# Kernel optimization log

Hardware: AMD Instinct MI355X
Metric: run time of the kernel (lower is better)

## Reference

```python
import jax, jax.numpy as jnp
import numpy as np

B = 1024      # number of states
NP = 32       # SVGD particles per state
AD = 20       # act_dim
OD = 64       # obs_dim
H = 256       # critic hidden width
STEPS = 5     # num_svgd_steps
LR = 0.1      # svgd_lr (adaptive_lr disabled)
SP0 = 1.0     # svgd_sigma_p0
ALIM = 1.0    # act_limit


def _q(obs, X, w1, b1, w2, b2, w3, b3):
    h = jnp.concatenate([obs, X], axis=-1)
    h = jax.nn.relu(h @ w1 + b1)
    h = jax.nn.relu(h @ w2 + b2)
    return jnp.squeeze(h @ w3 + b3, -1)


def _rbf(X):
    # X: [B, NP, AD] -> K [B,NP,NP], diff [B,NP,NP,AD], gamma [B,1,1], K_grad [B,NP,NP,AD]
    diff = X[:, :, None, :] - X[:, None, :, :]
    dist_sq = jnp.sum(diff * diff, axis=-1)
    # adaptive bandwidth via median heuristic (adaptive_sig=True)
    med = jnp.median(dist_sq.reshape(dist_sq.shape[0], -1), axis=-1)
    sig_sq = med / (2.0 * jnp.log(NP + 1.0))
    gamma = (1.0 / (2.0 * sig_sq + 1e-8))[:, None, None]
    K = jnp.exp(-gamma * dist_sq)
    K_grad = -2.0 * gamma[..., None] * diff * K[..., None]  # d/dx_i K(x_i, x_j)
    return K, diff, gamma, K_grad


def setup_inputs():
    key = jax.random.key(0)
    ks = jax.random.split(key, 16)
    N = B * NP

    def lin(k, fi, fo):
        return (jax.random.normal(k, (fi, fo), jnp.float32) / np.sqrt(fi)).astype(jnp.float32)

    return {
        "obs": jax.random.normal(ks[0], (N, OD), jnp.float32),
        "a0": jax.random.normal(ks[1], (N, AD), jnp.float32) * np.sqrt(SP0),
        "q1_w1": lin(ks[2], OD + AD, H), "q1_b1": jnp.zeros((H,), jnp.float32),
        "q1_w2": lin(ks[3], H, H),       "q1_b2": jnp.zeros((H,), jnp.float32),
        "q1_w3": lin(ks[4], H, 1),       "q1_b3": jnp.zeros((1,), jnp.float32),
        "q2_w1": lin(ks[5], OD + AD, H), "q2_b1": jnp.zeros((H,), jnp.float32),
        "q2_w2": lin(ks[6], H, H),       "q2_b2": jnp.zeros((H,), jnp.float32),
        "q2_w3": lin(ks[7], H, 1),       "q2_b3": jnp.zeros((1,), jnp.float32),
    }


def reference(obs, a0, q1_w1, q1_b1, q1_w2, q1_b2, q1_w3, q1_b3,
              q2_w1, q2_b1, q2_w2, q2_b2, q2_w3, q2_b3):
    eye = jnp.eye(NP, dtype=a0.dtype)

    def q_min_sum(Xf):
        q1 = _q(obs, Xf, q1_w1, q1_b1, q1_w2, q1_b2, q1_w3, q1_b3)
        q2 = _q(obs, Xf, q2_w1, q2_b1, q2_w2, q2_b2, q2_w3, q2_b3)
        return jnp.sum(jnp.minimum(q1, q2))

    score_fn = jax.grad(q_min_sum)  # autograd score function

    def step(carry, _):
        a, logp = carry
        score = score_fn(a).reshape(-1, NP, AD)                 # [B,NP,AD]
        X = a.reshape(-1, NP, AD)
        K, diff, gamma, Kg = _rbf(X)
        phi = (jnp.einsum('bij,bjd->bid', K, score) + Kg.sum(axis=1)) / NP
        # log-prob correction terms (with_logprob=True)
        term1 = jnp.mean(jnp.sum(Kg * score[:, None, :, :], axis=-1), axis=2)     # [B,NP]
        inner = jnp.sum(jnp.transpose(Kg, (0, 2, 1, 3)) * diff, axis=-1) \
                - AD * (K - eye)
        term2 = -2.0 * gamma[:, :, 0] * jnp.mean(inner, axis=1)                   # [B,NP]
        logp = logp - LR * (term1 + term2)
        a = a + LR * phi.reshape(a.shape)                        # svgd_optim
        return (a, logp), None

    logp0 = jnp.zeros((B, NP), a0.dtype)
    (a, logp_svgd), _ = jax.lax.scan(step, (a0, logp0), None, length=STEPS)

    a_sq = ALIM * jnp.tanh(a)                                    # [B*NP, AD]
    logp_normal = (-AD * 0.5 * jnp.log(2.0 * jnp.pi * SP0)
                   - 0.5 / SP0 * jnp.sum(a0 * a0, axis=-1)).reshape(-1, NP)
    logp_tanh = -jnp.sum(2.0 * (jnp.log(2.0) - a - jax.nn.softplus(-2.0 * a)),
                         axis=-1).reshape(-1, NP)
    logp_a = jnp.mean(logp_normal + logp_svgd + logp_tanh, axis=-1)  # [B]
    return a_sq, logp_a
```

## Files before the change

kernel.cpp:

```cpp
#include <hip/hip_runtime.h>
#include <math.h>

#define NPART 32
#define ADIM  20
#define ODIM  64
#define HID   256
#define NSTEPS 5
#define LRC   0.1f
#define NBLK  512
#define LOG33 3.4965075614664802f
#define A0LD  104

typedef short bf8 __attribute__((ext_vector_type(8)));
typedef short s4b __attribute__((ext_vector_type(4)));
typedef float f4  __attribute__((ext_vector_type(4)));
typedef unsigned u4 __attribute__((ext_vector_type(4)));

#define OW1T(n) ((n)*24576)
#define OW2T(n) (49152 + (n)*65536)
#define OW2C(n) (180224 + (n)*65536)
#define OW1X(n) (311296 + (n)*8192)
#define WS_ELEMS 327680

__device__ __forceinline__ short f2bf(float x) {
    unsigned u = __float_as_uint(x);
    u += 0x7FFFu + ((u >> 16) & 1u);
    return (short)(u >> 16);
}
__device__ __forceinline__ short f2bfT(float x) {
    return (short)(__float_as_uint(x) >> 16);
}
__device__ __forceinline__ float bf2f(short s) {
    return __uint_as_float(((unsigned)(unsigned short)s) << 16);
}

#define MFMA(a,b,c) __builtin_amdgcn_mfma_f32_16x16x32_bf16((a),(b),(c),0,0,0)

__global__ void prep_weights(const float* __restrict__ w1a, const float* __restrict__ w2a,
                             const float* __restrict__ w3a, const float* __restrict__ w1b,
                             const float* __restrict__ w2b, const float* __restrict__ w3b,
                             unsigned short* __restrict__ ws)
{
    int idx = blockIdx.x * 256 + threadIdx.x;
    if (idx >= WS_ELEMS) return;
    float val;
    if (idx < 49152) {
        int net = idx / 24576, rem = idx % 24576;
        int n = rem / 96, k = rem % 96;
        const float* w1 = net ? w1b : w1a;
        val = (k < 84) ? w1[k*256 + n] : 0.f;
    } else if (idx < 180224) {
        int t2 = idx - 49152; int net = t2 / 65536, rem = t2 % 65536;
        int n = rem / 256, k = rem % 256;
        const float* w2 = net ? w2b : w2a;
        val = w2[k*256 + n];
    } else if (idx < 311296) {
        int t2 = idx - 180224; int net = t2 / 65536, rem = t2 % 65536;
        const float* w2 = net ? w2b : w2a;
        const float* w3 = net ? w3b : w3a;
        val = w2[rem] * w3[rem % 256];
    } else {
        int t2 = idx - 311296; int net = t2 / 8192, rem = t2 % 8192;
        int d = rem / 256, n = rem % 256;
        const float* w1 = net ? w1b : w1a;
        val = (d < 20) ? w1[(64 + d)*256 + n] : 0.f;
    }
    ws[idx] = (unsigned short)f2bf(val);
}

__global__ void __launch_bounds__(512, 4)
svgd_main(const float* __restrict__ obs,  const float* __restrict__ a0g,
          const float* __restrict__ b1a,  const float* __restrict__ b2a, const float* __restrict__ b3a,
          const float* __restrict__ b1b,  const float* __restrict__ b2b, const float* __restrict__ b3b,
          const float* __restrict__ w3af, const float* __restrict__ w3bf,
          const unsigned short* __restrict__ ws, float* __restrict__ out)
{
    __shared__ __align__(16) short A0s[64*A0LD];
    __shared__ __align__(16) short hbuf[64*264];
    __shared__ unsigned maskS[2][2][64][8];
    __shared__ float Xm[64*20];
    __shared__ float scoreS[64*21];
    __shared__ float qpart[2][8][64];
    __shared__ int   winsS[64];
    __shared__ float logps[64];
    __shared__ unsigned short lutI[496], lutJ[496];
    __shared__ float med2[4];
    __shared__ float qvS[64];
    __shared__ float normsS[64], rowKS[64];
    __shared__ __align__(16) float diagS[64];

    float* d2sF = (float*)hbuf;
    float* GSF  = ((float*)hbuf) + 2304;
    short* SBs  = hbuf + 9216;
    short* KbS  = hbuf + 9216;
    short* STbS = hbuf + 11776;
    short* XTbS = hbuf + 14336;

    const int t = threadIdx.x, b = blockIdx.x;
    const int lane = t & 63, wv = t >> 6;
    const int q = lane >> 4, mp = lane & 15;
    const int nb = wv * 32;

    for (int p = t; p < 64*ODIM; p += 512) {
        int i = p >> 6, d = p & 63;
        A0s[i*A0LD + d] = f2bfT(obs[(b*64 + i)*ODIM + d]);
    }
    for (int p = t; p < 64*ADIM; p += 512) {
        int i = p / 20, d = p - i*20;
        float v = a0g[(b*64 + i)*20 + d];
        Xm[p] = v;
        A0s[i*A0LD + 64 + d] = f2bfT(v);
    }
    for (int p = t; p < 64*12; p += 512) { int i = p/12, d = p - i*12; A0s[i*A0LD + 84 + d] = 0; }
    if (t < 496) {
        int i_ = 0, rem = t;
        while (rem >= 31 - i_) { rem -= 31 - i_; ++i_; }
        lutI[t] = (unsigned short)i_; lutJ[t] = (unsigned short)(i_ + 1 + rem);
    }
    if (t < 64) logps[t] = 0.f;
    __syncthreads();

    for (int step = 0; step < NSTEPS; ++step) {
        for (int net = 0; net < 2; ++net) {
            const unsigned short* w1t = ws + OW1T(net);
            const unsigned short* w2t = ws + OW2T(net);
            const float* b1p = net ? b1b : b1a;
            const float* b2p = net ? b2b : b2a;
            const float* w3p = net ? w3bf : w3af;

            f4 acc[4][2];
            #pragma unroll
            for (int h = 0; h < 4; ++h) { acc[h][0] = (f4){0,0,0,0}; acc[h][1] = (f4){0,0,0,0}; }
            {
                const unsigned short* bp0 = w1t + (size_t)(nb +      mp)*96 + q*8;
                const unsigned short* bp1 = w1t + (size_t)(nb + 16 + mp)*96 + q*8;
                bf8 bb0 = *(const bf8*)bp0, bb1 = *(const bf8*)bp1;
                #pragma unroll
                for (int k0 = 0; k0 < 96; k0 += 32) {
                    bf8 n0 = bb0, n1 = bb1;
                    if (k0 + 32 < 96) { n0 = *(const bf8*)(bp0 + k0 + 32); n1 = *(const bf8*)(bp1 + k0 + 32); }
                    #pragma unroll
                    for (int h = 0; h < 4; ++h) {
                        bf8 aa = *(const bf8*)&A0s[(h*16 + mp)*A0LD + k0 + q*8];
                        acc[h][0] = MFMA(aa, bb0, acc[h][0]);
                        acc[h][1] = MFMA(aa, bb1, acc[h][1]);
                    }
                    bb0 = n0; bb1 = n1;
                }
            }
            {
                float bias0 = b1p[nb + mp], bias1 = b1p[nb + 16 + mp];
                #pragma unroll
                for (int h = 0; h < 4; ++h) {
                    #pragma unroll
                    for (int r = 0; r < 4; ++r) {
                        float v0 = acc[h][0][r] + bias0;
                        float v1 = acc[h][1][r] + bias1;
                        bool p0 = v0 > 0.f, p1 = v1 > 0.f;
                        unsigned long long bal0 = __ballot(p0);
                        unsigned long long bal1 = __ballot(p1);
                        int row = h*16 + q*4 + r;
                        hbuf[row*264 + nb +      mp] = f2bfT(p0 ? v0 : 0.f);
                        hbuf[row*264 + nb + 16 + mp] = f2bfT(p1 ? v1 : 0.f);
                        if (mp == 0) {
                            unsigned w = (unsigned)((bal0 >> (q*16)) & 0xFFFFull)
                                       | (((unsigned)((bal1 >> (q*16)) & 0xFFFFull)) << 16);
                            maskS[net][0][row][wv] = w;
                        }
                    }
                }
            }
            __syncthreads();

            #pragma unroll
            for (int h = 0; h < 4; ++h) { acc[h][0] = (f4){0,0,0,0}; acc[h][1] = (f4){0,0,0,0}; }
            {
                const unsigned short* bp0 = w2t + (size_t)(nb +      mp)*256 + q*8;
                const unsigned short* bp1 = w2t + (size_t)(nb + 16 + mp)*256 + q*8;
                bf8 bb0 = *(const bf8*)bp0, bb1 = *(const bf8*)bp1;
                #pragma unroll
                for (int k0 = 0; k0 < 256; k0 += 32) {
                    bf8 n0 = bb0, n1 = bb1;
                    if (k0 + 32 < 256) { n0 = *(const bf8*)(bp0 + k0 + 32); n1 = *(const bf8*)(bp1 + k0 + 32); }
                    #pragma unroll
                    for (int h = 0; h < 4; ++h) {
                        bf8 aa = *(const bf8*)&hbuf[(h*16 + mp)*264 + k0 + q*8];
                        acc[h][0] = MFMA(aa, bb0, acc[h][0]);
                        acc[h][1] = MFMA(aa, bb1, acc[h][1]);
                    }
                    bb0 = n0; bb1 = n1;
                }
            }
            {
                float bias0 = b2p[nb + mp], bias1 = b2p[nb + 16 + mp];
                float w30   = w3p[nb + mp], w31   = w3p[nb + 16 + mp];
                float qp[4][4] = {{0,0,0,0},{0,0,0,0},{0,0,0,0},{0,0,0,0}};
                #pragma unroll
                for (int h = 0; h < 4; ++h) {
                    #pragma unroll
                    for (int r = 0; r < 4; ++r) {
                        float v0 = acc[h][0][r] + bias0;
                        float v1 = acc[h][1][r] + bias1;
                        bool p0 = v0 > 0.f, p1 = v1 > 0.f;
                        unsigned long long bal0 = __ballot(p0);
                        unsigned long long bal1 = __ballot(p1);
                        if (mp == 0) {
                            unsigned w = (unsigned)((bal0 >> (q*16)) & 0xFFFFull)
                                       | (((unsigned)((bal1 >> (q*16)) & 0xFFFFull)) << 16);
                            maskS[net][1][h*16 + q*4 + r][wv] = w;
                        }
                        qp[h][r] += (p0 ? v0 * w30 : 0.f) + (p1 ? v1 * w31 : 0.f);
                    }
                }
                #pragma unroll
                for (int d = 1; d < 16; d <<= 1)
                    #pragma unroll
                    for (int h = 0; h < 4; ++h)
                        #pragma unroll
                        for (int r = 0; r < 4; ++r)
                            qp[h][r] += __shfl_xor(qp[h][r], d, 64);
                if (mp == 0) {
                    #pragma unroll
                    for (int h = 0; h < 4; ++h)
                        #pragma unroll
                        for (int r = 0; r < 4; ++r)
                            qpart[net][wv][h*16 + q*4 + r] = qp[h][r];
                }
            }
            __syncthreads();
        }

        if (t < 64) {
            float q0 = b3a[0], q1 = b3b[0];
            #pragma unroll
            for (int w = 0; w < 8; ++w) { q0 += qpart[0][w][t]; q1 += qpart[1][w][t]; }
            winsS[t] = (q0 <= q1) ? 0 : 1;
        }
        __syncthreads();

        for (int net = 0; net < 2; ++net) {
            const unsigned short* w2c = ws + OW2C(net);

            f4 acc[4][2];
            #pragma unroll
            for (int h = 0; h < 4; ++h) { acc[h][0] = (f4){0,0,0,0}; acc[h][1] = (f4){0,0,0,0}; }
            int win[4];
            #pragma unroll
            for (int h = 0; h < 4; ++h) win[h] = (winsS[h*16 + mp] == net);
            {
                const unsigned short* bp0 = w2c + (size_t)(nb +      mp)*256 + q*8;
                const unsigned short* bp1 = w2c + (size_t)(nb + 16 + mp)*256 + q*8;
                bf8 bb0 = *(const bf8*)bp0, bb1 = *(const bf8*)bp1;
                #pragma unroll
                for (int k0 = 0; k0 < 256; k0 += 32) {
                    bf8 n0 = bb0, n1 = bb1;
                    if (k0 + 32 < 256) { n0 = *(const bf8*)(bp0 + k0 + 32); n1 = *(const bf8*)(bp1 + k0 + 32); }
                    #pragma unroll
                    for (int h = 0; h < 4; ++h) {
                        unsigned bits = win[h] ? ((maskS[net][1][h*16 + mp][k0 >> 5] >> (q*8)) & 0xFFu) : 0u;
                        u4 mw;
                        mw[0] = ((bits &   1u) ? 0x3F80u : 0u) | ((bits &   2u) ? 0x3F800000u : 0u);
                        mw[1] = ((bits &   4u) ? 0x3F80u : 0u) | ((bits &   8u) ? 0x3F800000u : 0u);
                        mw[2] = ((bits &  16u) ? 0x3F80u : 0u) | ((bits &  32u) ? 0x3F800000u : 0u);
                        mw[3] = ((bits &  64u) ? 0x3F80u : 0u) | ((bits & 128u) ? 0x3F800000u : 0u);
                        bf8 aa = __builtin_bit_cast(bf8, mw);
                        acc[h][0] = MFMA(aa, bb0, acc[h][0]);
                        acc[h][1] = MFMA(aa, bb1, acc[h][1]);
                    }
                    bb0 = n0; bb1 = n1;
                }
            }
            #pragma unroll
            for (int h = 0; h < 4; ++h) {
                #pragma unroll
                for (int s = 0; s < 2; ++s) {
                    int col = nb + s*16 + mp;
                    #pragma unroll
                    for (int r = 0; r < 4; ++r) {
                        int row = h*16 + q*4 + r;
                        bool on = (maskS[net][0][row][col >> 5] >> (col & 31)) & 1u;
                        hbuf[row*264 + col] = f2bfT(on ? acc[h][s][r] : 0.f);
                    }
                }
            }
            __syncthreads();
            {
                int mt = wv & 3, ch = wv >> 2;
                const unsigned short* w1x = ws + OW1X(net);
                const unsigned short* bp  = w1x + (size_t)(ch*16 + mp)*256 + q*8;
                f4 sa = (f4){0,0,0,0};
                bf8 bx = *(const bf8*)bp;
                #pragma unroll
                for (int k0 = 0; k0 < 256; k0 += 32) {
                    bf8 nx = bx;
                    if (k0 + 32 < 256) nx = *(const bf8*)(bp + k0 + 32);
                    bf8 aa = *(const bf8*)&hbuf[(mt*16 + mp)*264 + k0 + q*8];
                    sa = MFMA(aa, bx, sa);
                    bx = nx;
                }
                int colD = ch*16 + mp;
                if (colD < 20) {
                    #pragma unroll
                    for (int r = 0; r < 4; ++r) {
                        int row = mt*16 + q*4 + r;
                        if (net == 0) scoreS[row*21 + colD]  = sa[r];
                        else          scoreS[row*21 + colD] += sa[r];
                    }
                }
            }
            __syncthreads();
        }

        if (t < 64) {
            int st = t >> 5;
            float nrm = 0.f, dg = 0.f;
            #pragma unroll
            for (int d = 0; d < 20; ++d) {
                float xb = bf2f(A0s[t*A0LD + 64 + d]);
                nrm += xb * xb;
                float sv = scoreS[t*21 + d];
                float xv = Xm[t*20 + d];
                dg += xv * sv;
                short sb = f2bfT(sv);
                SBs[t*40 + d] = sb;
                STbS[st*1280 + d*40 + (t & 31)] = sb;
                XTbS[st*1280 + d*40 + (t & 31)] = f2bfT(xv);
            }
            #pragma unroll
            for (int d = 20; d < 32; ++d) SBs[t*40 + d] = 0;
            normsS[t] = nrm;
            diagS[t]  = dg;
        }
        __syncthreads();

        {
            int stw = wv >> 2, mt = (wv >> 1) & 1, nt = wv & 1;
            bf8 aa  = *(const bf8*)&A0s[(stw*32 + mt*16 + mp)*A0LD + 64 + q*8];
            bf8 bbx = *(const bf8*)&A0s[(stw*32 + nt*16 + mp)*A0LD + 64 + q*8];
            bf8 bbs = *(const bf8*)&SBs[(stw*32 + nt*16 + mp)*40 + q*8];
            f4 gx = MFMA(aa, bbx, ((f4){0,0,0,0}));
            f4 gs = MFMA(aa, bbs, ((f4){0,0,0,0}));
            int jl = nt*16 + mp;
            float nj = normsS[stw*32 + jl];
            #pragma unroll
            for (int r = 0; r < 4; ++r) {
                int il = mt*16 + q*4 + r;
                d2sF[stw*1152 + il*36 + jl] = normsS[stw*32 + il] + nj - 2.f*gx[r];
                GSF [stw*1152 + il*36 + jl] = gs[r];
            }
        }
        __syncthreads();

        if (wv < 2) {
            const float* base = d2sF + wv*1152;
            float v[8];
            #pragma unroll
            for (int i = 0; i < 8; ++i) {
                int e = lane*8 + i;
                v[i] = (e < 496) ? base[lutI[e]*36 + lutJ[e]] : 3.4e38f;
            }
            for (int k = 2; k <= 512; k <<= 1) {
                for (int jj = k >> 1; jj >= 8; jj >>= 1) {
                    int lm = jj >> 3;
                    #pragma unroll
                    for (int i = 0; i < 8; ++i) {
                        float w = __shfl_xor(v[i], lm, 64);
                        int p = lane*8 + i;
                        bool takeMin = (((p & k) == 0) == ((p & jj) == 0));
                        v[i] = takeMin ? fminf(v[i], w) : fmaxf(v[i], w);
                    }
                }
                int jj0 = (k >> 1) < 4 ? (k >> 1) : 4;
                for (int jj = jj0; jj >= 1; jj >>= 1) {
                    #pragma unroll
                    for (int i = 0; i < 8; ++i) {
                        if ((i & jj) == 0) {
                            int i2 = i | jj;
                            int p = lane*8 + i;
                            bool up = ((p & k) == 0);
                            float x = v[i], y = v[i2];
                            float mn = fminf(x, y), mx = fmaxf(x, y);
                            v[i] = up ? mn : mx; v[i2] = up ? mx : mn;
                        }
                    }
                }
            }
            if (lane == 29) med2[wv*2 + 0] = v[7];
            if (lane == 30) med2[wv*2 + 1] = v[0];
        }
        __syncthreads();

        {
            int i = t >> 3, stw = i >> 5, il = i & 31, j0 = (t & 7) * 4;
            float medv = 0.5f * (med2[stw*2] + med2[stw*2 + 1]);
            float gam  = 1.f / (2.f * (medv / (2.f * LOG33)) + 1e-8f);
            f4 d2 = *(const f4*)&d2sF[stw*1152 + il*36 + j0];
            f4 gs = *(const f4*)&GSF [stw*1152 + il*36 + j0];
            f4 dg = *(const f4*)&diagS[stw*32 + j0];
            float K0 = expf(-gam * d2[0]), K1 = expf(-gam * d2[1]);
            float K2 = expf(-gam * d2[2]), K3 = expf(-gam * d2[3]);
            s4b kb; kb[0] = f2bfT(K0); kb[1] = f2bfT(K1); kb[2] = f2bfT(K2); kb[3] = f2bfT(K3);
            *(s4b*)&KbS[stw*1280 + il*40 + j0] = kb;
            float sK   = K0 + K1 + K2 + K3;
            float sKGS = K0*gs[0] + K1*gs[1] + K2*gs[2] + K3*gs[3];
            float sKd2 = K0*d2[0] + K1*d2[1] + K2*d2[2] + K3*d2[3];
            float sKdg = K0*dg[0] + K1*dg[1] + K2*dg[2] + K3*dg[3];
            #pragma unroll
            for (int d = 1; d < 8; d <<= 1) {
                sK   += __shfl_xor(sK,   d, 64);
                sKGS += __shfl_xor(sKGS, d, 64);
                sKd2 += __shfl_xor(sKd2, d, 64);
                sKdg += __shfl_xor(sKdg, d, 64);
            }
            if ((t & 7) == 0) {
                rowKS[i] = sK;
                float sdots = sKGS - sKdg;
                float ssum  = -2.f*gam*sdots
                              - 2.f*gam*(2.f*gam*sKd2 - 20.f*(sK - 1.f));
                logps[i] -= LRC * (ssum * (1.f/32.f));
            }
        }
        __syncthreads();

        {
            int stw = wv >> 2, mt = (wv >> 1) & 1, nt = wv & 1;
            float medv = 0.5f * (med2[stw*2] + med2[stw*2 + 1]);
            float gam  = 1.f / (2.f * (medv / (2.f * LOG33)) + 1e-8f);
            bf8 aa  = *(const bf8*)&KbS [stw*1280 + (mt*16 + mp)*40 + q*8];
            bf8 b1v = *(const bf8*)&STbS[stw*1280 + (nt*16 + mp)*40 + q*8];
            bf8 b2v = *(const bf8*)&XTbS[stw*1280 + (nt*16 + mp)*40 + q*8];
            f4 ks = MFMA(aa, b1v, ((f4){0,0,0,0}));
            f4 kx = MFMA(aa, b2v, ((f4){0,0,0,0}));
            int dd = nt*16 + mp;
            if (dd < 20) {
                #pragma unroll
                for (int r = 0; r < 4; ++r) {
                    int gi = stw*32 + mt*16 + q*4 + r;
                    float xi  = Xm[gi*20 + dd];
                    float phi = (ks[r] + 2.f*gam*(xi*rowKS[gi] - kx[r])) * (1.f/32.f);
                    float nx  = xi + LRC * phi;
                    Xm[gi*20 + dd] = nx;
                    A0s[gi*A0LD + 64 + dd] = f2bfT(nx);
                }
            }
        }
        __syncthreads();
    }

    for (int p = t; p < 64*20; p += 512) {
        int i = p / 20, d = p - i*20;
        out[(b*64 + i)*20 + d] = tanhf(Xm[p]);
    }
    if (t < 64) {
        float lt = 0.f, s0 = 0.f;
        for (int d = 0; d < 20; ++d) {
            float a  = Xm[t*20 + d];
            float x  = -2.f * a;
            float sp = fmaxf(x, 0.f) + log1pf(expf(-fabsf(x)));
            lt -= 2.f * (0.69314718056f - a - sp);
            float v = a0g[(b*64 + t)*20 + d];
            s0 += v * v;
        }
        qvS[t] = -18.3787706641f - 0.5f*s0 + logps[t] + lt;
    }
    __syncthreads();
    if (t < 2) {
        float s = 0.f;
        for (int i = 0; i < 32; ++i) s += qvS[t*32 + i];
        out[1024*32*20 + b*2 + t] = s * (1.f/32.f);
    }
}

extern "C" void kernel_launch(void* const* d_in, const int* in_sizes, int n_in,
                              void* d_out, int out_size, void* d_ws, size_t ws_size,
                              hipStream_t stream) {
    unsigned short* ws = (unsigned short*)d_ws;
    prep_weights<<<(WS_ELEMS + 255)/256, 256, 0, stream>>>(
        (const float*)d_in[2],  (const float*)d_in[4],  (const float*)d_in[6],
        (const float*)d_in[8],  (const float*)d_in[10], (const float*)d_in[12], ws);
    svgd_main<<<NBLK, 512, 0, stream>>>(
        (const float*)d_in[0],  (const float*)d_in[1],
        (const float*)d_in[3],  (const float*)d_in[5],  (const float*)d_in[7],
        (const float*)d_in[9],  (const float*)d_in[11], (const float*)d_in[13],
        (const float*)d_in[6],  (const float*)d_in[12],
        ws, (float*)d_out);
}
```

Baseline: 488.5 us.

## Parallelize per-row serial sections across all threads and drop a barrier

The winner-selection step is now computed redundantly in registers by every thread instead of by 64 threads into shared memory, which removes one __syncthreads. The per-particle norm/score-packing pass and the final log-prob pass are spread across all 512 threads (8 per row) with shuffle reductions instead of 64 threads looping serially. expf is replaced with the fast __expf intrinsic, and the mask array gets a padded stride to reduce bank conflicts. These target serial tails where most of the block sits idle, at the cost of redundant shared reads and slightly lower exp accuracy.

```diff
diff --git a/kernel.cpp b/kernel.cpp
--- a/kernel.cpp
+++ b/kernel.cpp
@@ -77,11 +77,10 @@
 {
     __shared__ __align__(16) short A0s[64*A0LD];
     __shared__ __align__(16) short hbuf[64*264];
-    __shared__ unsigned maskS[2][2][64][8];
+    __shared__ unsigned maskS[2][2][64][9];
     __shared__ float Xm[64*20];
     __shared__ float scoreS[64*21];
     __shared__ float qpart[2][8][64];
-    __shared__ int   winsS[64];
     __shared__ float logps[64];
     __shared__ unsigned short lutI[496], lutJ[496];
     __shared__ float med2[4];
@@ -230,23 +229,25 @@
             __syncthreads();
         }
 
-        if (t < 64) {
-            float q0 = b3a[0], q1 = b3b[0];
-            #pragma unroll
-            for (int w = 0; w < 8; ++w) { q0 += qpart[0][w][t]; q1 += qpart[1][w][t]; }
-            winsS[t] = (q0 <= q1) ? 0 : 1;
-        }
-        __syncthreads();
-
+        int winf[2][4];
+        {
+            float ba = b3a[0], bb_ = b3b[0];
+            #pragma unroll
+            for (int h = 0; h < 4; ++h) {
+                int row = h*16 + mp;
+                float q0 = ba, q1 = bb_;
+                #pragma unroll
+                for (int w = 0; w < 8; ++w) { q0 += qpart[0][w][row]; q1 += qpart[1][w][row]; }
+                winf[0][h] = (q0 <= q1) ? 1 : 0;
+                winf[1][h] = 1 - winf[0][h];
+            }
+        }
         for (int net = 0; net < 2; ++net) {
             const unsigned short* w2c = ws + OW2C(net);
 
             f4 acc[4][2];
             #pragma unroll
             for (int h = 0; h < 4; ++h) { acc[h][0] = (f4){0,0,0,0}; acc[h][1] = (f4){0,0,0,0}; }
-            int win[4];
-            #pragma unroll
-            for (int h = 0; h < 4; ++h) win[h] = (winsS[h*16 + mp] == net);
             {
                 const unsigned short* bp0 = w2c + (size_t)(nb +      mp)*256 + q*8;
                 const unsigned short* bp1 = w2c + (size_t)(nb + 16 + mp)*256 + q*8;
@@ -257,7 +258,7 @@
                     if (k0 + 32 < 256) { n0 = *(const bf8*)(bp0 + k0 + 32); n1 = *(const bf8*)(bp1 + k0 + 32); }
                     #pragma unroll
                     for (int h = 0; h < 4; ++h) {
-                        unsigned bits = win[h] ? ((maskS[net][1][h*16 + mp][k0 >> 5] >> (q*8)) & 0xFFu) : 0u;
+                        unsigned bits = winf[net][h] ? ((maskS[net][1][h*16 + mp][k0 >> 5] >> (q*8)) & 0xFFu) : 0u;
                         u4 mw;
                         mw[0] = ((bits &   1u) ? 0x3F80u : 0u) | ((bits &   2u) ? 0x3F800000u : 0u);
                         mw[1] = ((bits &   4u) ? 0x3F80u : 0u) | ((bits &   8u) ? 0x3F800000u : 0u);
@@ -311,25 +312,32 @@
             __syncthreads();
         }
 
-        if (t < 64) {
-            int st = t >> 5;
+        {
+            int i = t >> 3, j = t & 7, st = i >> 5;
             float nrm = 0.f, dg = 0.f;
             #pragma unroll
-            for (int d = 0; d < 20; ++d) {
-                float xb = bf2f(A0s[t*A0LD + 64 + d]);
-                nrm += xb * xb;
-                float sv = scoreS[t*21 + d];
-                float xv = Xm[t*20 + d];
-                dg += xv * sv;
-                short sb = f2bfT(sv);
-                SBs[t*40 + d] = sb;
-                STbS[st*1280 + d*40 + (t & 31)] = sb;
-                XTbS[st*1280 + d*40 + (t & 31)] = f2bfT(xv);
-            }
-            #pragma unroll
-            for (int d = 20; d < 32; ++d) SBs[t*40 + d] = 0;
-            normsS[t] = nrm;
-            diagS[t]  = dg;
+            for (int dd = 0; dd < 3; ++dd) {
+                int d = j + dd*8;
+                if (d < 20) {
+                    float xb = bf2f(A0s[i*A0LD + 64 + d]);
+                    nrm += xb * xb;
+                    float sv = scoreS[i*21 + d];
+                    float xv = Xm[i*20 + d];
+                    dg += xv * sv;
+                    short sb = f2bfT(sv);
+                    SBs[i*40 + d] = sb;
+                    STbS[st*1280 + d*40 + (i & 31)] = sb;
+                    XTbS[st*1280 + d*40 + (i & 31)] = f2bfT(xv);
+                }
+            }
+            SBs[i*40 + 20 + j] = 0;
+            if (j < 4) SBs[i*40 + 28 + j] = 0;
+            #pragma unroll
+            for (int d = 1; d < 8; d <<= 1) {
+                nrm += __shfl_xor(nrm, d, 64);
+                dg  += __shfl_xor(dg,  d, 64);
+            }
+            if (j == 0) { normsS[i] = nrm; diagS[i] = dg; }
         }
         __syncthreads();
 
@@ -397,8 +405,8 @@
             f4 d2 = *(const f4*)&d2sF[stw*1152 + il*36 + j0];
             f4 gs = *(const f4*)&GSF [stw*1152 + il*36 + j0];
             f4 dg = *(const f4*)&diagS[stw*32 + j0];
-            float K0 = expf(-gam * d2[0]), K1 = expf(-gam * d2[1]);
-            float K2 = expf(-gam * d2[2]), K3 = expf(-gam * d2[3]);
+            float K0 = __expf(-gam * d2[0]), K1 = __expf(-gam * d2[1]);
+            float K2 = __expf(-gam * d2[2]), K3 = __expf(-gam * d2[3]);
             s4b kb; kb[0] = f2bfT(K0); kb[1] = f2bfT(K1); kb[2] = f2bfT(K2); kb[3] = f2bfT(K3);
             *(s4b*)&KbS[stw*1280 + il*40 + j0] = kb;
             float sK   = K0 + K1 + K2 + K3;
@@ -451,17 +459,27 @@
         int i = p / 20, d = p - i*20;
         out[(b*64 + i)*20 + d] = tanhf(Xm[p]);
     }
-    if (t < 64) {
+    {
+        int i = t >> 3, j = t & 7;
         float lt = 0.f, s0 = 0.f;
-        for (int d = 0; d < 20; ++d) {
-            float a  = Xm[t*20 + d];
-            float x  = -2.f * a;
-            float sp = fmaxf(x, 0.f) + log1pf(expf(-fabsf(x)));
-            lt -= 2.f * (0.69314718056f - a - sp);
-            float v = a0g[(b*64 + t)*20 + d];
-            s0 += v * v;
-        }
-        qvS[t] = -18.3787706641f - 0.5f*s0 + logps[t] + lt;
+        #pragma unroll
+        for (int dd = 0; dd < 3; ++dd) {
+            int d = j + dd*8;
+            if (d < 20) {
+                float a  = Xm[i*20 + d];
+                float x  = -2.f * a;
+                float sp = fmaxf(x, 0.f) + log1pf(__expf(-fabsf(x)));
+                lt -= 2.f * (0.69314718056f - a - sp);
+                float v = a0g[(b*64 + i)*20 + d];
+                s0 += v * v;
+            }
+        }
+        #pragma unroll
+        for (int d = 1; d < 8; d <<= 1) {
+            lt += __shfl_xor(lt, d, 64);
+            s0 += __shfl_xor(s0, d, 64);
+        }
+        if (j == 0) qvS[i] = -18.3787706641f - 0.5f*s0 + logps[i] + lt;
     }
     __syncthreads();
     if (t < 2) {
```

Result: no change. 491.0 us (+0.5%).
